# Optimization experiments

Hardware: AMD Instinct MI355X
Metric: run time of the kernel (lower is better)

Reference implementation:

```python
import jax, jax.numpy as jnp
import numpy as np

N_NODES = 100000
N_EDGES = 1600000
IN_DIM = 256
OUT_DIM = 128


def setup_inputs() -> dict:
    key = jax.random.key(0)
    k1, k2, k3, k4 = jax.random.split(key, 4)
    x = jax.random.normal(k1, (N_NODES, IN_DIM), dtype=jnp.float32)
    edge_list = jax.random.randint(k2, (2, N_EDGES), 0, N_NODES, dtype=jnp.int64)
    # xavier_uniform with gain=1.414
    gW = 1.414 * np.sqrt(6.0 / (IN_DIM + OUT_DIM))
    W = jax.random.uniform(k3, (IN_DIM, OUT_DIM), dtype=jnp.float32, minval=-gW, maxval=gW)
    ga = 1.414 * np.sqrt(6.0 / (2 * OUT_DIM + 1))
    a = jax.random.uniform(k4, (2 * OUT_DIM, 1), dtype=jnp.float32, minval=-ga, maxval=ga)
    return {"x": x, "edge_list": edge_list, "W": W, "a": a}


def reference(x, edge_list, W, a):
    N = x.shape[0]
    src, dst = edge_list[0], edge_list[1]
    h = x @ W  # [N, out_dim]
    # cat([h[src], h[dst]]) @ a  ==  h[src] @ a[:d] + h[dst] @ a[d:]
    d = h.shape[1]
    s_src = (h @ a[:d]).ravel()  # [N]
    s_dst = (h @ a[d:]).ravel()  # [N]
    e = jax.nn.leaky_relu(s_src[src] + s_dst[dst], negative_slope=0.2)  # [E]
    # sparse softmax over rows (segments = src node)
    seg_max = jax.ops.segment_max(e, src, num_segments=N)  # [N]
    ex = jnp.exp(e - seg_max[src])  # [E]
    denom = jax.ops.segment_sum(ex, src, num_segments=N)  # [N]
    attn = ex / jnp.where(denom > 0, denom, 1.0)[src]  # [E]
    # sparse aggregate: h_prime[i] = sum_{edges (i,j)} attn_ij * h[j]
    h_prime = jax.ops.segment_sum(attn[:, None] * h[dst], src, num_segments=N)  # [N, d]
    return jax.nn.elu(h_prime)
```

## Files before the change

kernel.cpp:

```cpp
#include <hip/hip_runtime.h>
#include <hip/hip_bf16.h>
#include <cstdint>
#include <cstddef>

#define NN 100000
#define NE 1600000
#define KD 256
#define OD 128
#define NB 391
#define CAP 8192
#define PCAP 9984
#define NGB 782

typedef __attribute__((ext_vector_type(8))) __bf16 bf16x8;
typedef __attribute__((ext_vector_type(4))) float f32x4;
typedef __attribute__((ext_vector_type(8))) unsigned short ushort8;

static __device__ __forceinline__ unsigned short f2bf(float f) {
  return __builtin_bit_cast(unsigned short, (__bf16)f);
}

__global__ void prep_wt_k(const float* __restrict__ W, unsigned short* __restrict__ Wt,
                          int* __restrict__ bcur) {
  const int i = blockIdx.x * 256 + threadIdx.x;
  const int k = i >> 7;
  const int n = i & 127;
  Wt[n * KD + k] = f2bf(W[i]);
  if (i < NB) bcur[i] = i * CAP;
}

__global__ __launch_bounds__(512, 4) void fused_k(
    const float* __restrict__ x, const unsigned short* __restrict__ Wt,
    const float* __restrict__ a, unsigned short* __restrict__ h,
    float* __restrict__ ssrc, float* __restrict__ sdst,
    const int* __restrict__ el, int* __restrict__ bcur,
    unsigned* __restrict__ stage) {
  __shared__ alignas(16) char smem[65536];
  const int t = threadIdx.x;

  if (blockIdx.x < NGB) {
    unsigned short* Bl = (unsigned short*)smem;
#pragma unroll
    for (int it = 0; it < 8; ++it) {
      const int c = it * 512 + t;
      const int r = c >> 5;
      const int c16 = c & 31;
      const ushort8 v = *(const ushort8*)(Wt + r * 256 + c16 * 8);
      const int byt = (r * 512 + c16 * 16) ^ ((r & 7) << 4);
      *(ushort8*)((char*)Bl + byt) = v;
    }
    const int lane = t & 63;
    const int wave = t >> 6;
    const int col = lane & 15;
    const int kg = lane >> 4;
    const int m0 = blockIdx.x * 128 + wave * 16;
    const int arow = m0 + col;
    const bool rowok = arow < NN;
    const float* __restrict__ xrow = x + (size_t)arow * KD;
    __syncthreads();

    f32x4 acc[8];
#pragma unroll
    for (int i = 0; i < 8; ++i) acc[i] = (f32x4)0.0f;

#pragma unroll
    for (int s = 0; s < 8; ++s) {
      const int kk = s * 32 + kg * 8;
      bf16x8 af = (bf16x8)(__bf16)0.0f;
      if (rowok) {
        const float4 f0 = *(const float4*)(xrow + kk);
        const float4 f1 = *(const float4*)(xrow + kk + 4);
        af[0] = (__bf16)f0.x; af[1] = (__bf16)f0.y; af[2] = (__bf16)f0.z; af[3] = (__bf16)f0.w;
        af[4] = (__bf16)f1.x; af[5] = (__bf16)f1.y; af[6] = (__bf16)f1.z; af[7] = (__bf16)f1.w;
      }
#pragma unroll
      for (int nt = 0; nt < 8; ++nt) {
        const int n = nt * 16 + col;
        const int byt = (n * 512 + s * 64 + kg * 16) ^ ((col & 7) << 4);
        const ushort8 bu = *(const ushort8*)((const char*)Bl + byt);
        const bf16x8 bf = __builtin_bit_cast(bf16x8, bu);
        acc[nt] = __builtin_amdgcn_mfma_f32_16x16x32_bf16(af, bf, acc[nt], 0, 0, 0);
      }
    }

    float ps[4] = {0.f, 0.f, 0.f, 0.f};
    float pd[4] = {0.f, 0.f, 0.f, 0.f};
#pragma unroll
    for (int nt = 0; nt < 8; ++nt) {
      const int n = nt * 16 + col;
      const float av = a[n];
      const float av2 = a[OD + n];
#pragma unroll
      for (int r = 0; r < 4; ++r) {
        const float v = acc[nt][r];
        const int row = m0 + kg * 4 + r;
        if (row < NN) h[(size_t)row * OD + n] = f2bf(v);
        ps[r] += v * av;
        pd[r] += v * av2;
      }
    }
#pragma unroll
    for (int off = 1; off < 16; off <<= 1) {
#pragma unroll
      for (int r = 0; r < 4; ++r) {
        ps[r] += __shfl_xor(ps[r], off, 64);
        pd[r] += __shfl_xor(pd[r], off, 64);
      }
    }
    if (col == 0) {
#pragma unroll
      for (int r = 0; r < 4; ++r) {
        const int row = m0 + kg * 4 + r;
        if (row < NN) {
          ssrc[row] = ps[r] * 1.442695041f;
          sdst[row] = pd[r] * 1.442695041f;
        }
      }
    }
  } else {
    unsigned* sorted = (unsigned*)smem;
    unsigned short* bkid = (unsigned short*)(smem + 16384);
    int* hist  = (int*)(smem + 24576);
    int* off   = (int*)(smem + 26144);
    int* cur   = (int*)(smem + 27712);
    int* delta = (int*)(smem + 29276);
    const int te = (blockIdx.x - NGB) * 4096 + t * 8;
    int s[8], d[8];
    bool valid[8];
#pragma unroll
    for (int u = 0; u < 8; ++u) valid[u] = (te + u) < NE;
    if (te + 7 < NE) {
      const int4 a0 = *(const int4*)(el + te);
      const int4 a1 = *(const int4*)(el + te + 4);
      const int4 b0 = *(const int4*)(el + NE + te);
      const int4 b1 = *(const int4*)(el + NE + te + 4);
      s[0] = a0.x; s[1] = a0.y; s[2] = a0.z; s[3] = a0.w;
      s[4] = a1.x; s[5] = a1.y; s[6] = a1.z; s[7] = a1.w;
      d[0] = b0.x; d[1] = b0.y; d[2] = b0.z; d[3] = b0.w;
      d[4] = b1.x; d[5] = b1.y; d[6] = b1.z; d[7] = b1.w;
    } else {
#pragma unroll
      for (int u = 0; u < 8; ++u) {
        s[u] = valid[u] ? el[te + u] : 0;
        d[u] = valid[u] ? el[NE + te + u] : 0;
      }
    }
    for (int i = t; i <= NB; i += 512) hist[i] = 0;
    __syncthreads();
#pragma unroll
    for (int u = 0; u < 8; ++u)
      if (valid[u]) atomicAdd(&hist[s[u] >> 8], 1);
    __syncthreads();
    if (t < 64) {
      int v[7];
      int sum = 0;
#pragma unroll
      for (int i = 0; i < 7; ++i) {
        const int idx = t * 7 + i;
        v[i] = (idx <= NB) ? hist[idx] : 0;
        sum += v[i];
      }
      int pre = sum;
#pragma unroll
      for (int o = 1; o < 64; o <<= 1) {
        const int nb = __shfl_up(pre, o, 64);
        if (t >= o) pre += nb;
      }
      pre -= sum;
      int run = pre;
#pragma unroll
      for (int i = 0; i < 7; ++i) {
        const int idx = t * 7 + i;
        if (idx <= NB) off[idx] = run;
        run += v[i];
      }
    }
    __syncthreads();
    for (int i = t; i < NB; i += 512) cur[i] = off[i];
    __syncthreads();
#pragma unroll
    for (int u = 0; u < 8; ++u)
      if (valid[u]) {
        const int b = s[u] >> 8;
        const int p = atomicAdd(&cur[b], 1);
        sorted[p] = ((unsigned)(s[u] & 255) << 17) | (unsigned)d[u];
        bkid[p] = (unsigned short)b;
      }
    __syncthreads();
    for (int b = t; b < NB; b += 512) {
      const int len = off[b + 1] - off[b];
      if (len > 0) {
        const int gb = atomicAdd(&bcur[b], len);
        delta[b] = gb - off[b];
      }
    }
    __syncthreads();
    const int n = off[NB];
    for (int i = t; i < n; i += 512) {
      const int b = bkid[i];
      const int pos = delta[b] + i;
      if (pos < (b + 1) * CAP) stage[pos] = sorted[i];
    }
  }
}

__global__ __launch_bounds__(256) void place2_k(const unsigned* __restrict__ stage,
                                                const int* __restrict__ bcur,
                                                const float* __restrict__ ssrc,
                                                const float* __restrict__ sdst,
                                                unsigned* __restrict__ csrw,
                                                uint2* __restrict__ rc) {
  __shared__ unsigned ebuf[CAP];
  __shared__ float sl[256];
  __shared__ int hist2[256];
  __shared__ int exc[256];
  __shared__ int cur2[256];
  __shared__ unsigned firstd[256];
  const int b = blockIdx.x;
  const int t = threadIdx.x;
  const int node = b * 256 + t;
  const int base = b * PCAP;
  int tot = bcur[b] - b * CAP;
  tot = tot > CAP ? CAP : tot;
  hist2[t] = 0;
  sl[t] = (node < NN) ? ssrc[node] : 0.f;
  for (int i = t; i < tot; i += 256) ebuf[i] = stage[(size_t)b * CAP + i];
  __syncthreads();
  for (int i = t; i < tot; i += 256) atomicAdd(&hist2[ebuf[i] >> 17], 1);
  __syncthreads();
  if (t < 64) {
    int p[4];
    int sum = 0;
#pragma unroll
    for (int i = 0; i < 4; ++i) {
      const int c = hist2[t * 4 + i];
      p[i] = (c + 7) & ~7;
      sum += p[i];
    }
    int pre = sum;
#pragma unroll
    for (int o = 1; o < 64; o <<= 1) {
      const int nb = __shfl_up(pre, o, 64);
      if (t >= o) pre += nb;
    }
    pre -= sum;
    int run = pre;
#pragma unroll
    for (int i = 0; i < 4; ++i) { exc[t * 4 + i] = run; run += p[i]; }
  }
  __syncthreads();
  const int c = hist2[t];
  const int pc = (c + 7) & ~7;
  if (node < NN) rc[node] = make_uint2((unsigned)pc, (unsigned)(base + exc[t]));
  cur2[t] = exc[t];
  __syncthreads();
  for (int i = t; i < tot; i += 256) {
    const unsigned u = ebuf[i];
    const int s = u >> 17;
    const unsigned d = u & 0x1ffffu;
    const float sv = sl[s] + sdst[d];
    const float w = exp2f(fmaxf(sv, 0.2f * sv));
    unsigned wb = __builtin_bit_cast(unsigned, w);
    wb += 0x7fffu + ((wb >> 16) & 1u);
    const unsigned ent = ((wb >> 16) << 17) | d;
    const int p = atomicAdd(&cur2[s], 1);
    if (p == exc[s]) firstd[s] = d;
    csrw[base + p] = ent;
  }
  __syncthreads();
  if (c > 0) {
    const unsigned padent = firstd[t];
    const int e0 = exc[t];
    for (int i = c; i < pc; ++i) csrw[base + e0 + i] = padent;
  }
}

__global__ __launch_bounds__(256) void aggr_k(
    const unsigned short* __restrict__ h, const unsigned* __restrict__ csrw,
    const uint2* __restrict__ rc, float* __restrict__ out) {
  const int lane = threadIdx.x & 63;
  const int g = lane >> 4;
  const int sub = lane & 15;
  const int node = blockIdx.x * 4 + (threadIdx.x >> 6);
  const uint2 rcv = rc[node];
  const int pdeg = (int)rcv.x;
  const int r0 = (int)rcv.y;
  const uint4* __restrict__ hp = (const uint4*)h;
  float acc[8] = {0.f, 0.f, 0.f, 0.f, 0.f, 0.f, 0.f, 0.f};
  float sw = 0.f;
  const unsigned losel = 0x05040100u;
  const unsigned hisel = 0x07060302u;
  const unsigned onepk = 0x3F803F80u;
  const int nit = pdeg >> 3;
  if (nit > 0) {
    int j = r0 + g;
    unsigned uA0 = csrw[j];
    unsigned uA1 = csrw[j + 4];
    uint4 pA0 = hp[(uA0 & 0x1ffffu) * 16u + sub];
    uint4 pA1 = hp[(uA1 & 0x1ffffu) * 16u + sub];
    for (int it = 0; it < nit; ++it) {
      unsigned uB0, uB1;
      uint4 pB0, pB1;
      const bool more = (it + 1) < nit;
      if (more) {
        j += 8;
        uB0 = csrw[j];
        uB1 = csrw[j + 4];
        pB0 = hp[(uB0 & 0x1ffffu) * 16u + sub];
        pB1 = hp[(uB1 & 0x1ffffu) * 16u + sub];
      }
      const unsigned wpk = (uA0 >> 17) | ((uA1 >> 17) << 16);
      asm("v_dot2_f32_bf16 %0, %1, %2, %0" : "+v"(sw) : "v"(wpk), "v"(onepk));
      const unsigned k0a[4] = {pA0.x, pA0.y, pA0.z, pA0.w};
      const unsigned k1a[4] = {pA1.x, pA1.y, pA1.z, pA1.w};
#pragma unroll
      for (int q = 0; q < 4; ++q) {
        const unsigned lo = __builtin_amdgcn_perm(k1a[q], k0a[q], losel);
        const unsigned hi = __builtin_amdgcn_perm(k1a[q], k0a[q], hisel);
        asm("v_dot2_f32_bf16 %0, %1, %2, %0" : "+v"(acc[q * 2]) : "v"(wpk), "v"(lo));
        asm("v_dot2_f32_bf16 %0, %1, %2, %0" : "+v"(acc[q * 2 + 1]) : "v"(wpk), "v"(hi));
      }
      if (more) { uA0 = uB0; uA1 = uB1; pA0 = pB0; pA1 = pB1; }
    }
  }
#pragma unroll
  for (int off = 16; off < 64; off <<= 1) {
    sw += __shfl_xor(sw, off, 64);
#pragma unroll
    for (int q = 0; q < 8; ++q) acc[q] += __shfl_xor(acc[q], off, 64);
  }
  const float inv = pdeg > 0 ? 1.0f / sw : 0.f;
  float o[8];
#pragma unroll
  for (int q = 0; q < 8; ++q) {
    const float v = acc[q] * inv;
    o[q] = v > 0.f ? v : __expf(v) - 1.f;
  }
  if (lane < 16) {
    float4* op = (float4*)(out + (size_t)node * OD + sub * 8);
    op[0] = make_float4(o[0], o[1], o[2], o[3]);
    op[1] = make_float4(o[4], o[5], o[6], o[7]);
  }
}

extern "C" void kernel_launch(void* const* d_in, const int* in_sizes, int n_in,
                              void* d_out, int out_size, void* d_ws, size_t ws_size,
                              hipStream_t stream) {
  const float* x = (const float*)d_in[0];
  const int* el = (const int*)d_in[1];
  const float* W = (const float*)d_in[2];
  const float* a = (const float*)d_in[3];
  float* out = (float*)d_out;
  char* ws = (char*)d_ws;

  const size_t S = 400384;
  float* ssrc    = (float*)(ws + 0 * S);
  float* sdst    = (float*)(ws + 1 * S);
  uint2* rc      = (uint2*)(ws + 2 * S);
  int* bcur      = (int*)(ws + 4 * S);
  unsigned short* Wt = (unsigned short*)(ws + 4 * S + 8192);
  unsigned short* h  = (unsigned short*)(ws + 4 * S + 8192 + 65536);
  unsigned* csrw = (unsigned*)(ws + 4 * S + 8192 + 65536 + (size_t)NN * OD * 2);
  unsigned* stage = (unsigned*)d_out;

  prep_wt_k<<<128, 256, 0, stream>>>(W, Wt, bcur);
  fused_k<<<NGB + NB, 512, 0, stream>>>(x, Wt, a, h, ssrc, sdst, el, bcur, stage);
  place2_k<<<NB, 256, 0, stream>>>(stage, bcur, ssrc, sdst, csrw, rc);
  aggr_k<<<NN / 4, 256, 0, stream>>>(h, csrw, rc, out);
}
```

Before: 119.4 us.

## Fuse edge placement and aggregation into one kernel with LDS-resident CSR

```diff
diff --git a/kernel.cpp b/kernel.cpp
--- a/kernel.cpp
+++ b/kernel.cpp
@@ -7,9 +7,9 @@
 #define NE 1600000
 #define KD 256
 #define OD 128
-#define NB 391
-#define CAP 8192
-#define PCAP 9984
+#define NB 782
+#define CAP 2560
+#define PCAPL 3456
 #define NGB 782
 
 typedef __attribute__((ext_vector_type(8))) __bf16 bf16x8;
@@ -121,9 +121,9 @@
     unsigned* sorted = (unsigned*)smem;
     unsigned short* bkid = (unsigned short*)(smem + 16384);
     int* hist  = (int*)(smem + 24576);
-    int* off   = (int*)(smem + 26144);
-    int* cur   = (int*)(smem + 27712);
-    int* delta = (int*)(smem + 29276);
+    int* off   = (int*)(smem + 27712);
+    int* cur   = (int*)(smem + 30848);
+    int* delta = (int*)(smem + 33984);
     const int te = (blockIdx.x - NGB) * 4096 + t * 8;
     int s[8], d[8];
     bool valid[8];
@@ -149,14 +149,14 @@
     __syncthreads();
 #pragma unroll
     for (int u = 0; u < 8; ++u)
-      if (valid[u]) atomicAdd(&hist[s[u] >> 8], 1);
+      if (valid[u]) atomicAdd(&hist[s[u] >> 7], 1);
     __syncthreads();
     if (t < 64) {
-      int v[7];
+      int v[13];
       int sum = 0;
 #pragma unroll
-      for (int i = 0; i < 7; ++i) {
-        const int idx = t * 7 + i;
+      for (int i = 0; i < 13; ++i) {
+        const int idx = t * 13 + i;
         v[i] = (idx <= NB) ? hist[idx] : 0;
         sum += v[i];
       }
@@ -169,8 +169,8 @@
       pre -= sum;
       int run = pre;
 #pragma unroll
-      for (int i = 0; i < 7; ++i) {
-        const int idx = t * 7 + i;
+      for (int i = 0; i < 13; ++i) {
+        const int idx = t * 13 + i;
         if (idx <= NB) off[idx] = run;
         run += v[i];
       }
@@ -181,9 +181,9 @@
 #pragma unroll
     for (int u = 0; u < 8; ++u)
       if (valid[u]) {
-        const int b = s[u] >> 8;
+        const int b = s[u] >> 7;
         const int p = atomicAdd(&cur[b], 1);
-        sorted[p] = ((unsigned)(s[u] & 255) << 17) | (unsigned)d[u];
+        sorted[p] = ((unsigned)(s[u] & 127) << 17) | (unsigned)d[u];
         bkid[p] = (unsigned short)b;
       }
     __syncthreads();
@@ -204,39 +204,35 @@
   }
 }
 
-__global__ __launch_bounds__(256) void place2_k(const unsigned* __restrict__ stage,
-                                                const int* __restrict__ bcur,
-                                                const float* __restrict__ ssrc,
-                                                const float* __restrict__ sdst,
-                                                unsigned* __restrict__ csrw,
-                                                uint2* __restrict__ rc) {
+__global__ __launch_bounds__(512, 4) void paggr_k(
+    const unsigned* __restrict__ stage, const int* __restrict__ bcur,
+    const float* __restrict__ ssrc, const float* __restrict__ sdst,
+    const unsigned short* __restrict__ h, float* __restrict__ out) {
   __shared__ unsigned ebuf[CAP];
-  __shared__ float sl[256];
-  __shared__ int hist2[256];
-  __shared__ int exc[256];
-  __shared__ int cur2[256];
-  __shared__ unsigned firstd[256];
+  __shared__ unsigned csrl[PCAPL];
+  __shared__ float sl[128];
+  __shared__ int hist2[128];
+  __shared__ int exc[128];
+  __shared__ int cur2[128];
+  __shared__ unsigned firstd[128];
+  __shared__ unsigned short pdegs[128];
   const int b = blockIdx.x;
   const int t = threadIdx.x;
-  const int node = b * 256 + t;
-  const int base = b * PCAP;
   int tot = bcur[b] - b * CAP;
   tot = tot > CAP ? CAP : tot;
-  hist2[t] = 0;
-  sl[t] = (node < NN) ? ssrc[node] : 0.f;
-  for (int i = t; i < tot; i += 256) ebuf[i] = stage[(size_t)b * CAP + i];
-  __syncthreads();
-  for (int i = t; i < tot; i += 256) atomicAdd(&hist2[ebuf[i] >> 17], 1);
+  if (t < 128) {
+    hist2[t] = 0;
+    const int node = b * 128 + t;
+    sl[t] = (node < NN) ? ssrc[node] : 0.f;
+  }
+  for (int i = t; i < tot; i += 512) ebuf[i] = stage[(size_t)b * CAP + i];
+  __syncthreads();
+  for (int i = t; i < tot; i += 512) atomicAdd(&hist2[ebuf[i] >> 17], 1);
   __syncthreads();
   if (t < 64) {
-    int p[4];
-    int sum = 0;
-#pragma unroll
-    for (int i = 0; i < 4; ++i) {
-      const int c = hist2[t * 4 + i];
-      p[i] = (c + 7) & ~7;
-      sum += p[i];
-    }
+    const int p0 = (hist2[t * 2] + 7) & ~7;
+    const int p1 = (hist2[t * 2 + 1] + 7) & ~7;
+    const int sum = p0 + p1;
     int pre = sum;
 #pragma unroll
     for (int o = 1; o < 64; o <<= 1) {
@@ -244,17 +240,16 @@
       if (t >= o) pre += nb;
     }
     pre -= sum;
-    int run = pre;
-#pragma unroll
-    for (int i = 0; i < 4; ++i) { exc[t * 4 + i] = run; run += p[i]; }
-  }
-  __syncthreads();
-  const int c = hist2[t];
-  const int pc = (c + 7) & ~7;
-  if (node < NN) rc[node] = make_uint2((unsigned)pc, (unsigned)(base + exc[t]));
-  cur2[t] = exc[t];
-  __syncthreads();
-  for (int i = t; i < tot; i += 256) {
+    exc[t * 2] = pre;
+    exc[t * 2 + 1] = pre + p0;
+  }
+  __syncthreads();
+  if (t < 128) {
+    cur2[t] = exc[t];
+    pdegs[t] = (unsigned short)((hist2[t] + 7) & ~7);
+  }
+  __syncthreads();
+  for (int i = t; i < tot; i += 512) {
     const unsigned u = ebuf[i];
     const int s = u >> 17;
     const unsigned d = u & 0x1ffffu;
@@ -262,57 +257,48 @@
     const float w = exp2f(fmaxf(sv, 0.2f * sv));
     unsigned wb = __builtin_bit_cast(unsigned, w);
     wb += 0x7fffu + ((wb >> 16) & 1u);
-    const unsigned ent = ((wb >> 16) << 17) | d;
     const int p = atomicAdd(&cur2[s], 1);
     if (p == exc[s]) firstd[s] = d;
-    csrw[base + p] = ent;
-  }
-  __syncthreads();
-  if (c > 0) {
-    const unsigned padent = firstd[t];
-    const int e0 = exc[t];
-    for (int i = c; i < pc; ++i) csrw[base + e0 + i] = padent;
-  }
-}
-
-__global__ __launch_bounds__(256) void aggr_k(
-    const unsigned short* __restrict__ h, const unsigned* __restrict__ csrw,
-    const uint2* __restrict__ rc, float* __restrict__ out) {
-  const int lane = threadIdx.x & 63;
+    csrl[p] = ((wb >> 16) << 17) | d;
+  }
+  __syncthreads();
+  if (t < 128) {
+    const int c = hist2[t];
+    const int pc = pdegs[t];
+    if (c > 0) {
+      const unsigned padent = firstd[t];
+      const int e0 = exc[t];
+      for (int i = c; i < pc; ++i) csrl[e0 + i] = padent;
+    }
+  }
+  __syncthreads();
+  const int lane = t & 63;
+  const int wave = t >> 6;
   const int g = lane >> 4;
   const int sub = lane & 15;
-  const int node = blockIdx.x * 4 + (threadIdx.x >> 6);
-  const uint2 rcv = rc[node];
-  const int pdeg = (int)rcv.x;
-  const int r0 = (int)rcv.y;
   const uint4* __restrict__ hp = (const uint4*)h;
-  float acc[8] = {0.f, 0.f, 0.f, 0.f, 0.f, 0.f, 0.f, 0.f};
-  float sw = 0.f;
   const unsigned losel = 0x05040100u;
   const unsigned hisel = 0x07060302u;
   const unsigned onepk = 0x3F803F80u;
-  const int nit = pdeg >> 3;
-  if (nit > 0) {
+  for (int k = 0; k < 16; ++k) {
+    const int ln = wave * 16 + k;
+    const int node = b * 128 + ln;
+    if (node >= NN) break;
+    const int pdeg = pdegs[ln];
+    const int r0 = exc[ln];
+    float acc[8] = {0.f, 0.f, 0.f, 0.f, 0.f, 0.f, 0.f, 0.f};
+    float sw = 0.f;
+    const int nit = pdeg >> 3;
     int j = r0 + g;
-    unsigned uA0 = csrw[j];
-    unsigned uA1 = csrw[j + 4];
-    uint4 pA0 = hp[(uA0 & 0x1ffffu) * 16u + sub];
-    uint4 pA1 = hp[(uA1 & 0x1ffffu) * 16u + sub];
-    for (int it = 0; it < nit; ++it) {
-      unsigned uB0, uB1;
-      uint4 pB0, pB1;
-      const bool more = (it + 1) < nit;
-      if (more) {
-        j += 8;
-        uB0 = csrw[j];
-        uB1 = csrw[j + 4];
-        pB0 = hp[(uB0 & 0x1ffffu) * 16u + sub];
-        pB1 = hp[(uB1 & 0x1ffffu) * 16u + sub];
-      }
-      const unsigned wpk = (uA0 >> 17) | ((uA1 >> 17) << 16);
+    for (int it = 0; it < nit; ++it, j += 8) {
+      const unsigned u0 = csrl[j];
+      const unsigned u1 = csrl[j + 4];
+      const uint4 p0 = hp[(u0 & 0x1ffffu) * 16u + sub];
+      const uint4 p1 = hp[(u1 & 0x1ffffu) * 16u + sub];
+      const unsigned wpk = (u0 >> 17) | ((u1 >> 17) << 16);
       asm("v_dot2_f32_bf16 %0, %1, %2, %0" : "+v"(sw) : "v"(wpk), "v"(onepk));
-      const unsigned k0a[4] = {pA0.x, pA0.y, pA0.z, pA0.w};
-      const unsigned k1a[4] = {pA1.x, pA1.y, pA1.z, pA1.w};
+      const unsigned k0a[4] = {p0.x, p0.y, p0.z, p0.w};
+      const unsigned k1a[4] = {p1.x, p1.y, p1.z, p1.w};
 #pragma unroll
       for (int q = 0; q < 4; ++q) {
         const unsigned lo = __builtin_amdgcn_perm(k1a[q], k0a[q], losel);
@@ -320,26 +306,25 @@
         asm("v_dot2_f32_bf16 %0, %1, %2, %0" : "+v"(acc[q * 2]) : "v"(wpk), "v"(lo));
         asm("v_dot2_f32_bf16 %0, %1, %2, %0" : "+v"(acc[q * 2 + 1]) : "v"(wpk), "v"(hi));
       }
-      if (more) { uA0 = uB0; uA1 = uB1; pA0 = pB0; pA1 = pB1; }
-    }
-  }
-#pragma unroll
-  for (int off = 16; off < 64; off <<= 1) {
-    sw += __shfl_xor(sw, off, 64);
-#pragma unroll
-    for (int q = 0; q < 8; ++q) acc[q] += __shfl_xor(acc[q], off, 64);
-  }
-  const float inv = pdeg > 0 ? 1.0f / sw : 0.f;
-  float o[8];
-#pragma unroll
-  for (int q = 0; q < 8; ++q) {
-    const float v = acc[q] * inv;
-    o[q] = v > 0.f ? v : __expf(v) - 1.f;
-  }
-  if (lane < 16) {
-    float4* op = (float4*)(out + (size_t)node * OD + sub * 8);
-    op[0] = make_float4(o[0], o[1], o[2], o[3]);
-    op[1] = make_float4(o[4], o[5], o[6], o[7]);
+    }
+#pragma unroll
+    for (int off = 16; off < 64; off <<= 1) {
+      sw += __shfl_xor(sw, off, 64);
+#pragma unroll
+      for (int q = 0; q < 8; ++q) acc[q] += __shfl_xor(acc[q], off, 64);
+    }
+    const float inv = pdeg > 0 ? 1.0f / sw : 0.f;
+    float o[8];
+#pragma unroll
+    for (int q = 0; q < 8; ++q) {
+      const float v = acc[q] * inv;
+      o[q] = v > 0.f ? v : __expf(v) - 1.f;
+    }
+    if (lane < 16) {
+      float4* op = (float4*)(out + (size_t)node * OD + sub * 8);
+      op[0] = make_float4(o[0], o[1], o[2], o[3]);
+      op[1] = make_float4(o[4], o[5], o[6], o[7]);
+    }
   }
 }
 
@@ -356,15 +341,12 @@
   const size_t S = 400384;
   float* ssrc    = (float*)(ws + 0 * S);
   float* sdst    = (float*)(ws + 1 * S);
-  uint2* rc      = (uint2*)(ws + 2 * S);
-  int* bcur      = (int*)(ws + 4 * S);
-  unsigned short* Wt = (unsigned short*)(ws + 4 * S + 8192);
-  unsigned short* h  = (unsigned short*)(ws + 4 * S + 8192 + 65536);
-  unsigned* csrw = (unsigned*)(ws + 4 * S + 8192 + 65536 + (size_t)NN * OD * 2);
-  unsigned* stage = (unsigned*)d_out;
+  int* bcur      = (int*)(ws + 2 * S);
+  unsigned short* Wt = (unsigned short*)(ws + 2 * S + 8192);
+  unsigned short* h  = (unsigned short*)(ws + 2 * S + 8192 + 65536);
+  unsigned* stage = (unsigned*)(ws + 2 * S + 8192 + 65536 + (size_t)NN * OD * 2);
 
   prep_wt_k<<<128, 256, 0, stream>>>(W, Wt, bcur);
   fused_k<<<NGB + NB, 512, 0, stream>>>(x, Wt, a, h, ssrc, sdst, el, bcur, stage);
-  place2_k<<<NB, 256, 0, stream>>>(stage, bcur, ssrc, sdst, csrw, rc);
-  aggr_k<<<NN / 4, 256, 0, stream>>>(h, csrw, rc, out);
-}
+  paggr_k<<<NB, 512, 0, stream>>>(stage, bcur, ssrc, sdst, h, out);
+}
```

Result: slower. 123.7 us (+3.6%).
